# Optimization experiments

Hardware: AMD Instinct MI355X
Metric: run time of the kernel (lower is better)

## Reference

```python
import jax, jax.numpy as jnp
import numpy as np

D_MODEL = 1024
N_HEADS = 16
HEAD_DIM = D_MODEL // N_HEADS


def setup_inputs() -> dict:
    key = jax.random.key(0)
    ks = jax.random.split(key, 9)
    B, S = 2, 2048
    s = 1.0 / np.sqrt(D_MODEL)
    return {
        "x": jax.random.normal(ks[0], (B, S, D_MODEL), dtype=jnp.float32),
        "Wq": jax.random.normal(ks[1], (D_MODEL, D_MODEL), dtype=jnp.float32) * s,
        "bq": jnp.zeros((D_MODEL,), dtype=jnp.float32),
        "Wk": jax.random.normal(ks[2], (D_MODEL, D_MODEL), dtype=jnp.float32) * s,
        "bk": jnp.zeros((D_MODEL,), dtype=jnp.float32),
        "Wv": jax.random.normal(ks[3], (D_MODEL, D_MODEL), dtype=jnp.float32) * s,
        "bv": jnp.zeros((D_MODEL,), dtype=jnp.float32),
        "Wo": jax.random.normal(ks[4], (D_MODEL, D_MODEL), dtype=jnp.float32) * s,
        "bo": jnp.zeros((D_MODEL,), dtype=jnp.float32),
    }


def _rope_emb(seq_len, dtype):
    # inv_freq over even dims of head_dim; emb = cat(freqs, freqs)
    inv_freq = 1.0 / (10000.0 ** (jnp.arange(0, HEAD_DIM, 2, dtype=jnp.float32) / HEAD_DIM))
    t = jnp.arange(seq_len, dtype=jnp.float32)
    freqs = t[:, None] * inv_freq[None, :]          # [S, head_dim/2]
    emb = jnp.concatenate([freqs, freqs], axis=-1)  # [S, head_dim]
    return emb.astype(dtype)[None, None, :, :]       # [1,1,S,head_dim]


def _rotate_half(x):
    x1, x2 = jnp.split(x, 2, axis=-1)
    return jnp.concatenate([-x2, x1], axis=-1)


def _apply_rope(x, emb):
    return x * jnp.cos(emb) + _rotate_half(x) * jnp.sin(emb)


def reference(x, Wq, bq, Wk, bk, Wv, bv, Wo, bo):
    B, S, _ = x.shape
    # projections (torch Linear: x @ W.T + b; here W is stored already as [in,out])
    q = (x @ Wq + bq).reshape(B, S, N_HEADS, HEAD_DIM).transpose(0, 2, 1, 3)
    k = (x @ Wk + bk).reshape(B, S, N_HEADS, HEAD_DIM).transpose(0, 2, 1, 3)
    v = (x @ Wv + bv).reshape(B, S, N_HEADS, HEAD_DIM).transpose(0, 2, 1, 3)
    emb = _rope_emb(S, x.dtype)
    q = _apply_rope(q, emb)
    k = _apply_rope(k, emb)
    scores = jnp.einsum('bhqd,bhkd->bhqk', q, k) / jnp.sqrt(jnp.asarray(HEAD_DIM, x.dtype))
    attn = jax.nn.softmax(scores, axis=-1)
    out = jnp.einsum('bhqk,bhkd->bhqd', attn, v)
    out = out.transpose(0, 2, 1, 3).reshape(B, S, D_MODEL)
    return out @ Wo + bo
```

## Files before the change

### kernel.cpp

```cpp
#include <hip/hip_runtime.h>
#include <hip/hip_bf16.h>
#include <math.h>

#define SEQ 2048
#define DM 1024
#define NH 16
#define HD 64
#define NBH 32
#define MTOT 4096

typedef __attribute__((ext_vector_type(8))) short short8;
typedef __attribute__((ext_vector_type(4))) float floatx4;
typedef __attribute__((ext_vector_type(8))) unsigned short u16x8;

__device__ __forceinline__ unsigned short f2bf(float f) {
    unsigned int u = __float_as_uint(f);
    u += 0x7FFFu + ((u >> 16) & 1u);
    return (unsigned short)(u >> 16);
}

#define AS1C const __attribute__((address_space(1))) void*
#define AS3  __attribute__((address_space(3))) void*

#define QSCALE 0.18033688011112042f

__global__ __launch_bounds__(256) void cvt_x_kernel(
    const float* __restrict__ x, unsigned short* __restrict__ xb)
{
    size_t base = ((size_t)blockIdx.x * 256 + threadIdx.x) * 8;
    float4 a = *(const float4*)(x + base);
    float4 b = *(const float4*)(x + base + 4);
    u16x8 o;
    o[0]=f2bf(a.x); o[1]=f2bf(a.y); o[2]=f2bf(a.z); o[3]=f2bf(a.w);
    o[4]=f2bf(b.x); o[5]=f2bf(b.y); o[6]=f2bf(b.z); o[7]=f2bf(b.w);
    *(u16x8*)(xb + base) = o;
}

__global__ __launch_bounds__(256) void cvt_w_kernel(
    const float* __restrict__ Wq, const float* __restrict__ Wk,
    const float* __restrict__ Wv, const float* __restrict__ Wo,
    unsigned short* __restrict__ Wt)
{
    __shared__ float Ls[64][65];
    const int z = blockIdx.z;
    const float* src = (z==0) ? Wq : (z==1) ? Wk : (z==2) ? Wv : Wo;
    unsigned short* dst = Wt + (size_t)z * DM * DM;
    const int tid = threadIdx.x;
    const int k0 = blockIdx.x * 64, n0 = blockIdx.y * 64;

    int r = tid >> 2, cseg = (tid & 3) * 16;
    #pragma unroll
    for (int e = 0; e < 4; ++e) {
        float4 v = *(const float4*)(src + (size_t)(k0 + r) * DM + n0 + cseg + e*4);
        Ls[r][cseg+e*4+0] = v.x; Ls[r][cseg+e*4+1] = v.y;
        Ls[r][cseg+e*4+2] = v.z; Ls[r][cseg+e*4+3] = v.w;
    }
    __syncthreads();
    int n = tid >> 2, kseg = (tid & 3) * 16;
    #pragma unroll
    for (int half = 0; half < 2; ++half) {
        u16x8 o;
        #pragma unroll
        for (int e = 0; e < 8; ++e) o[e] = f2bf(Ls[kseg + half*8 + e][n]);
        *(u16x8*)(dst + (size_t)(n0 + n) * DM + k0 + kseg + half*8) = o;
    }
}

#define GEMM_CORE(A_, Bt_, m0_, n0_)                                          \
    const int tid = threadIdx.x;                                              \
    const int wave = tid >> 6, lane = tid & 63;                               \
    const int quad = lane >> 4, l16 = lane & 15;                              \
    const int mh = (wave & 1) * 64, nh = (wave >> 1) * 64;                    \
    floatx4 acc[4][4];                                                        \
    _Pragma("unroll")                                                         \
    for (int i = 0; i < 4; ++i)                                               \
        _Pragma("unroll")                                                     \
        for (int j = 0; j < 4; ++j) acc[i][j] = (floatx4){0.f,0.f,0.f,0.f};   \
    {                                                                         \
        const int srow = wave*32 + (lane>>2);                                 \
        const int scol = (lane & 3) * 8;                                      \
        const unsigned short* ga = A_ + (size_t)(m0_ + srow)*DM + scol;       \
        const unsigned short* gb = Bt_ + (size_t)(n0_ + srow)*DM + scol;      \
        char* lA = (char*)As; char* lB = (char*)Bs;                           \
        for (int k0 = 0; k0 < DM; k0 += 32) {                                 \
            __syncthreads();                                                  \
            _Pragma("unroll")                                                 \
            for (int u = 0; u < 2; ++u) {                                     \
                __builtin_amdgcn_global_load_lds(                             \
                    (AS1C)(ga + (size_t)u*16*DM + k0),                        \
                    (AS3)(lA + (wave*32 + u*16)*64), 16, 0, 0);               \
                __builtin_amdgcn_global_load_lds(                             \
                    (AS1C)(gb + (size_t)u*16*DM + k0),                        \
                    (AS3)(lB + (wave*32 + u*16)*64), 16, 0, 0);               \
            }                                                                 \
            __syncthreads();                                                  \
            short8 af[4], bf[4];                                              \
            _Pragma("unroll")                                                 \
            for (int t = 0; t < 4; ++t) {                                     \
                af[t] = *(const short8*)&As[(mh + t*16 + l16)*32 + quad*8];   \
                bf[t] = *(const short8*)&Bs[(nh + t*16 + l16)*32 + quad*8];   \
            }                                                                 \
            _Pragma("unroll")                                                 \
            for (int mt = 0; mt < 4; ++mt)                                    \
                _Pragma("unroll")                                             \
                for (int nt = 0; nt < 4; ++nt)                                \
                    acc[mt][nt] = __builtin_amdgcn_mfma_f32_16x16x32_bf16(    \
                        af[mt], bf[nt], acc[mt][nt], 0, 0, 0);                \
        }                                                                     \
    }

__global__ __launch_bounds__(256, 3) void qkv_gemm_kernel(
    const unsigned short* __restrict__ xb, const unsigned short* __restrict__ Wt,
    const float* __restrict__ bq, const float* __restrict__ bk,
    const float* __restrict__ bv,
    unsigned short* __restrict__ qb, unsigned short* __restrict__ kb,
    unsigned short* __restrict__ vtg)
{
    __shared__ unsigned short As[128*32];
    __shared__ unsigned short Bs[128*32];
    const int z = blockIdx.z;
    const unsigned short* Bt = Wt + (size_t)z * DM * DM;
    const float* bias = (z==0) ? bq : (z==1) ? bk : bv;
    const int m0 = blockIdx.x * 128, n0 = blockIdx.y * 128;

    GEMM_CORE(xb, Bt, m0, n0)

    float bb[4];
    #pragma unroll
    for (int nt = 0; nt < 4; ++nt) bb[nt] = bias[n0 + nh + nt*16 + l16];

    if (z == 2) {
        unsigned short* Tw = (wave & 1) ? Bs : As;
        const int b = m0 >> 11;
        const int bufsel = tid >> 7, nl = tid & 127;
        const int ng = n0 + nl, hh = ng >> 6, dhh = ng & 63;
        unsigned short* vrow = vtg + ((size_t)((b*NH + hh)*HD + dhh))*SEQ;
        #pragma unroll
        for (int t = 0; t < 4; ++t) {
            __syncthreads();
            #pragma unroll
            for (int nt = 0; nt < 4; ++nt)
                #pragma unroll
                for (int r = 0; r < 4; ++r)
                    Tw[(nh + nt*16 + l16)*24 + quad*4 + r] =
                        f2bf(acc[t][nt][r] + bb[nt]);
            __syncthreads();
            const unsigned short* T2 = bufsel ? Bs : As;
            int sbase = (m0 & 2047) + bufsel*64 + t*16;
            u16x8 lo = *(const u16x8*)&T2[nl*24];
            u16x8 hi = *(const u16x8*)&T2[nl*24 + 8];
            *(u16x8*)(vrow + sbase)     = lo;
            *(u16x8*)(vrow + sbase + 8) = hi;
        }
    } else {
        unsigned short* outh = (z==0) ? qb : kb;
        const float scl = (z == 0) ? QSCALE : 1.0f;
        float inv[2];
        #pragma unroll
        for (int p = 0; p < 2; ++p)
            inv[p] = __expf(-(float)(p*16 + l16) * 0.28782313662425572f);
        #pragma unroll
        for (int mt = 0; mt < 4; ++mt)
            #pragma unroll
            for (int r = 0; r < 4; ++r) {
                int m = m0 + mh + mt*16 + quad*4 + r;
                int b = m >> 11, s = m & (SEQ-1);
                #pragma unroll
                for (int p = 0; p < 2; ++p) {
                    float fr = (float)s * inv[p];
                    float sn, c; __sincosf(fr, &sn, &c);
                    int n1 = n0 + nh + p*16 + l16;
                    int h = n1 >> 6, dh = n1 & 63;
                    float v1 = acc[mt][p  ][r] + bb[p];
                    float v2 = acc[mt][p+2][r] + bb[p+2];
                    unsigned short* base = outh + ((size_t)(b*NH + h)*SEQ + s)*HD;
                    base[dh]      = f2bf((v1*c - v2*sn) * scl);
                    base[dh + 32] = f2bf((v2*c + v1*sn) * scl);
                }
            }
    }
}

__global__ __launch_bounds__(256, 3) void out_gemm_kernel(
    const unsigned short* __restrict__ ctxb, const unsigned short* __restrict__ Wto,
    const float* __restrict__ bo, float* __restrict__ outf)
{
    __shared__ unsigned short As[128*32];
    __shared__ unsigned short Bs[128*32];
    const int m0 = blockIdx.x * 128, n0 = blockIdx.y * 128;

    GEMM_CORE(ctxb, Wto, m0, n0)

    float bb[4];
    #pragma unroll
    for (int nt = 0; nt < 4; ++nt) bb[nt] = bo[n0 + nh + nt*16 + l16];
    #pragma unroll
    for (int mt = 0; mt < 4; ++mt)
        #pragma unroll
        for (int r = 0; r < 4; ++r) {
            int m = m0 + mh + mt*16 + quad*4 + r;
            #pragma unroll
            for (int nt = 0; nt < 4; ++nt) {
                int n = n0 + nh + nt*16 + l16;
                outf[(size_t)m*DM + n] = acc[mt][nt][r] + bb[nt];
            }
        }
}

#define LSTP 72
__global__ __launch_bounds__(512, 4) void attn_mfma_kernel(
    const unsigned short* __restrict__ Q, const unsigned short* __restrict__ K,
    const unsigned short* __restrict__ Vtg, unsigned short* __restrict__ ctxb)
{
    __shared__ unsigned short Ks[2*64*32];
    __shared__ unsigned short Vt[2*64*32];
    __shared__ unsigned short Ps[8*16*LSTP];

    const int tid  = threadIdx.x;
    const int wave = tid >> 6, lane = tid & 63;
    const int quad = lane >> 4, l16 = lane & 15;
    const int qt = blockIdx.x, bh = blockIdx.y;

    const unsigned short* Qb = Q + (size_t)bh * SEQ * HD;
    const unsigned short* Kb = K + (size_t)bh * SEQ * HD;
    const unsigned short* Vb = Vtg + (size_t)bh * HD * SEQ;

    short8 qf[2];
    {
        const unsigned short* qrow = Qb + (size_t)(qt*128 + wave*16 + l16)*HD;
        qf[0] = *(const short8*)(qrow + quad*8);
        qf[1] = *(const short8*)(qrow + 32 + quad*8);
    }

    const unsigned short* gsrc0; const unsigned short* gsrc1;
    char* ldst0; char* ldst1;
    int step;
    {
        const int ib = (wave & 3) * 2;
        int f0 = (ib+0)*512 + lane*8;
        int f1 = (ib+1)*512 + lane*8;
        int ch0 = f0>>11, row0 = (f0&2047)>>5, g0 = ((f0>>3)&3) ^ (row0&3);
        int ch1 = f1>>11, row1 = (f1&2047)>>5, g1 = ((f1>>3)&3) ^ (row1&3);
        if (wave < 4) {
            gsrc0 = Kb + (size_t)row0*HD + ch0*32 + g0*8;
            gsrc1 = Kb + (size_t)row1*HD + ch1*32 + g1*8;
            ldst0 = (char*)Ks + (ib+0)*1024;
            ldst1 = (char*)Ks + (ib+1)*1024;
            step = 64*HD;
        } else {
            gsrc0 = Vb + (size_t)row0*SEQ + ch0*32 + g0*8;
            gsrc1 = Vb + (size_t)row1*SEQ + ch1*32 + g1*8;
            ldst0 = (char*)Vt + (ib+0)*1024;
            ldst1 = (char*)Vt + (ib+1)*1024;
            step = 64;
        }
    }

    float l_i[4];
    floatx4 Oacc[4];
    #pragma unroll
    for (int r = 0; r < 4; ++r) l_i[r] = 0.f;
    #pragma unroll
    for (int dt = 0; dt < 4; ++dt) Oacc[dt] = (floatx4){0.f,0.f,0.f,0.f};

    const int swz8 = (quad ^ (l16&3)) * 8;

    for (int kt = 0; kt < SEQ/64; ++kt) {
        __syncthreads();
        __builtin_amdgcn_global_load_lds((AS1C)gsrc0, (AS3)ldst0, 16, 0, 0);
        __builtin_amdgcn_global_load_lds((AS1C)gsrc1, (AS3)ldst1, 16, 0, 0);
        gsrc0 += step; gsrc1 += step;
        __syncthreads();

        floatx4 Sacc[4];
        #pragma unroll
        for (int c = 0; c < 4; ++c) Sacc[c] = (floatx4){0.f,0.f,0.f,0.f};
        #pragma unroll
        for (int s = 0; s < 2; ++s) {
            #pragma unroll
            for (int c = 0; c < 4; ++c) {
                short8 b = *(const short8*)&Ks[s*2048 + (c*16+l16)*32 + swz8];
                Sacc[c] = __builtin_amdgcn_mfma_f32_16x16x32_bf16(qf[s], b, Sacc[c], 0, 0, 0);
            }
        }

        #pragma unroll
        for (int r = 0; r < 4; ++r) {
            float p0 = exp2f(Sacc[0][r]);
            float p1 = exp2f(Sacc[1][r]);
            float p2 = exp2f(Sacc[2][r]);
            float p3 = exp2f(Sacc[3][r]);
            l_i[r] += (p0 + p1) + (p2 + p3);
            __hip_bfloat162 w0 = __float22bfloat162_rn(make_float2(p0, p1));
            __hip_bfloat162 w1 = __float22bfloat162_rn(make_float2(p2, p3));
            unsigned short* prow = &Ps[(wave*16 + quad*4 + r)*LSTP + l16];
            __builtin_memcpy(&prow[0],  &w0.x, 2);
            __builtin_memcpy(&prow[16], &w0.y, 2);
            __builtin_memcpy(&prow[32], &w1.x, 2);
            __builtin_memcpy(&prow[48], &w1.y, 2);
        }

        #pragma unroll
        for (int s = 0; s < 2; ++s) {
            short8 a = *(const short8*)&Ps[(wave*16 + l16)*LSTP + s*32 + quad*8];
            #pragma unroll
            for (int dt = 0; dt < 4; ++dt) {
                short8 b = *(const short8*)&Vt[s*2048 + (dt*16+l16)*32 + swz8];
                Oacc[dt] = __builtin_amdgcn_mfma_f32_16x16x32_bf16(a, b, Oacc[dt], 0, 0, 0);
            }
        }
    }

    #pragma unroll
    for (int mask = 1; mask < 16; mask <<= 1)
        #pragma unroll
        for (int r = 0; r < 4; ++r)
            l_i[r] += __shfl_xor(l_i[r], mask);

    int b = bh >> 4, h = bh & 15;
    #pragma unroll
    for (int r = 0; r < 4; ++r) {
        int sr = qt*128 + wave*16 + quad*4 + r;
        float invl = 1.0f / l_i[r];
        unsigned short* dst = ctxb + ((size_t)(b*SEQ + sr))*DM + h*HD;
        #pragma unroll
        for (int dt = 0; dt < 4; ++dt)
            dst[dt*16 + l16] = f2bf(Oacc[dt][r] * invl);
    }
}

extern "C" void kernel_launch(void* const* d_in, const int* in_sizes, int n_in,
                              void* d_out, int out_size, void* d_ws, size_t ws_size,
                              hipStream_t stream) {
    const float* x  = (const float*)d_in[0];
    const float* Wq = (const float*)d_in[1];
    const float* bq = (const float*)d_in[2];
    const float* Wk = (const float*)d_in[3];
    const float* bk = (const float*)d_in[4];
    const float* Wv = (const float*)d_in[5];
    const float* bv = (const float*)d_in[6];
    const float* Wo = (const float*)d_in[7];
    const float* bo = (const float*)d_in[8];
    float* out = (float*)d_out;

    char* ws = (char*)d_ws;
    unsigned short* xb   = (unsigned short*)(ws);
    unsigned short* Wt   = (unsigned short*)(ws +  8u*1024*1024);
    unsigned short* qb   = (unsigned short*)(ws + 16u*1024*1024);
    unsigned short* kb   = (unsigned short*)(ws + 24u*1024*1024);
    unsigned short* vtg  = (unsigned short*)(ws + 32u*1024*1024);
    unsigned short* ctxb = (unsigned short*)(ws + 40u*1024*1024);

    cvt_x_kernel<<<(MTOT*DM/8)/256, 256, 0, stream>>>(x, xb);
    cvt_w_kernel<<<dim3(DM/64, DM/64, 4), 256, 0, stream>>>(Wq, Wk, Wv, Wo, Wt);

    qkv_gemm_kernel<<<dim3(MTOT/128, DM/128, 3), 256, 0, stream>>>(
        xb, Wt, bq, bk, bv, qb, kb, vtg);

    attn_mfma_kernel<<<dim3(SEQ/128, NBH), 512, 0, stream>>>(qb, kb, vtg, ctxb);

    out_gemm_kernel<<<dim3(MTOT/128, DM/128), 256, 0, stream>>>(
        ctxb, Wt + (size_t)3*DM*DM, bo, out);
    (void)in_sizes; (void)n_in; (void)out_size; (void)ws_size;
}
```

Before: 216.0 us.

## Widen attention key tile to 128, permute Q/K head layout, vectorize RoPE stores

The attention kernel now processes 128 keys per iteration instead of 64. This halves the number of barrier-separated load phases, and the P matrix is permuted in LDS to match. The QKV epilogue writes Q/K with a permuted head-dim layout (pairs interleaved), so each lane emits one 8-byte vector store instead of scattered 2-byte stores. This works because the dot product is invariant when Q and K are permuted the same way. The grid is flattened so the 32 heads of one query tile launch adjacently. The larger tile raises LDS and register use, which could lower occupancy.

Measured after the change: 212.0 us. No clear change (-1.8%).

```diff
diff --git a/kernel.cpp b/kernel.cpp
--- a/kernel.cpp
+++ b/kernel.cpp
@@ -12,6 +12,7 @@
 typedef __attribute__((ext_vector_type(8))) short short8;
 typedef __attribute__((ext_vector_type(4))) float floatx4;
 typedef __attribute__((ext_vector_type(8))) unsigned short u16x8;
+typedef __attribute__((ext_vector_type(4))) unsigned short u16x4;
 
 __device__ __forceinline__ unsigned short f2bf(float f) {
     unsigned int u = __float_as_uint(f);
@@ -155,28 +156,28 @@
     } else {
         unsigned short* outh = (z==0) ? qb : kb;
         const float scl = (z == 0) ? QSCALE : 1.0f;
-        float inv[2];
-        #pragma unroll
-        for (int p = 0; p < 2; ++p)
-            inv[p] = __expf(-(float)(p*16 + l16) * 0.28782313662425572f);
+        const int h = (n0 + nh) >> 6;
+        float inv0 = __expf(-(float)l16        * 0.28782313662425572f);
+        float inv1 = __expf(-(float)(l16 + 16) * 0.28782313662425572f);
         #pragma unroll
         for (int mt = 0; mt < 4; ++mt)
             #pragma unroll
             for (int r = 0; r < 4; ++r) {
                 int m = m0 + mh + mt*16 + quad*4 + r;
                 int b = m >> 11, s = m & (SEQ-1);
-                #pragma unroll
-                for (int p = 0; p < 2; ++p) {
-                    float fr = (float)s * inv[p];
-                    float sn, c; __sincosf(fr, &sn, &c);
-                    int n1 = n0 + nh + p*16 + l16;
-                    int h = n1 >> 6, dh = n1 & 63;
-                    float v1 = acc[mt][p  ][r] + bb[p];
-                    float v2 = acc[mt][p+2][r] + bb[p+2];
-                    unsigned short* base = outh + ((size_t)(b*NH + h)*SEQ + s)*HD;
-                    base[dh]      = f2bf((v1*c - v2*sn) * scl);
-                    base[dh + 32] = f2bf((v2*c + v1*sn) * scl);
-                }
+                float s0, c0, s1, c1;
+                __sincosf((float)s * inv0, &s0, &c0);
+                __sincosf((float)s * inv1, &s1, &c1);
+                float a0 = acc[mt][0][r] + bb[0];
+                float a1 = acc[mt][1][r] + bb[1];
+                float a2 = acc[mt][2][r] + bb[2];
+                float a3 = acc[mt][3][r] + bb[3];
+                u16x4 o;
+                o[0] = f2bf((a0*c0 - a2*s0) * scl);
+                o[1] = f2bf((a1*c1 - a3*s1) * scl);
+                o[2] = f2bf((a2*c0 + a0*s0) * scl);
+                o[3] = f2bf((a3*c1 + a1*s1) * scl);
+                *(u16x4*)(outh + ((size_t)((b*NH + h)*SEQ + s))*HD + 4*l16) = o;
             }
     }
 }
@@ -212,14 +213,15 @@
     const unsigned short* __restrict__ Q, const unsigned short* __restrict__ K,
     const unsigned short* __restrict__ Vtg, unsigned short* __restrict__ ctxb)
 {
-    __shared__ unsigned short Ks[2*64*32];
-    __shared__ unsigned short Vt[2*64*32];
+    __shared__ unsigned short Ks[2*128*32];
+    __shared__ unsigned short Vt[4*64*32];
     __shared__ unsigned short Ps[8*16*LSTP];
 
     const int tid  = threadIdx.x;
     const int wave = tid >> 6, lane = tid & 63;
     const int quad = lane >> 4, l16 = lane & 15;
-    const int qt = blockIdx.x, bh = blockIdx.y;
+    const int bh = blockIdx.x & 31;
+    const int qt = blockIdx.x >> 5;
 
     const unsigned short* Qb = Q + (size_t)bh * SEQ * HD;
     const unsigned short* Kb = K + (size_t)bh * SEQ * HD;
@@ -232,27 +234,31 @@
         qf[1] = *(const short8*)(qrow + 32 + quad*8);
     }
 
-    const unsigned short* gsrc0; const unsigned short* gsrc1;
-    char* ldst0; char* ldst1;
+    const unsigned short* gsrc[4];
+    char* ldst[4];
     int step;
     {
-        const int ib = (wave & 3) * 2;
-        int f0 = (ib+0)*512 + lane*8;
-        int f1 = (ib+1)*512 + lane*8;
-        int ch0 = f0>>11, row0 = (f0&2047)>>5, g0 = ((f0>>3)&3) ^ (row0&3);
-        int ch1 = f1>>11, row1 = (f1&2047)>>5, g1 = ((f1>>3)&3) ^ (row1&3);
+        const int idx = (wave & 3)*64 + lane;
         if (wave < 4) {
-            gsrc0 = Kb + (size_t)row0*HD + ch0*32 + g0*8;
-            gsrc1 = Kb + (size_t)row1*HD + ch1*32 + g1*8;
-            ldst0 = (char*)Ks + (ib+0)*1024;
-            ldst1 = (char*)Ks + (ib+1)*1024;
-            step = 64*HD;
+            #pragma unroll
+            for (int u = 0; u < 4; ++u) {
+                int fI = u*2048 + idx*8;
+                int s  = fI >> 12, rm = fI & 4095;
+                int key = rm >> 5, g = ((rm >> 3) & 3) ^ (key & 3);
+                gsrc[u] = Kb + (size_t)key*HD + s*32 + g*8;
+                ldst[u] = (char*)Ks + (u*2048 + (wave & 3)*512)*2;
+            }
+            step = 128*HD;
         } else {
-            gsrc0 = Vb + (size_t)row0*SEQ + ch0*32 + g0*8;
-            gsrc1 = Vb + (size_t)row1*SEQ + ch1*32 + g1*8;
-            ldst0 = (char*)Vt + (ib+0)*1024;
-            ldst1 = (char*)Vt + (ib+1)*1024;
-            step = 64;
+            #pragma unroll
+            for (int u = 0; u < 4; ++u) {
+                int fI = u*2048 + idx*8;
+                int ch = fI >> 11, rm = fI & 2047;
+                int d = rm >> 5, g = ((rm >> 3) & 3) ^ (d & 3);
+                gsrc[u] = Vb + (size_t)d*SEQ + ch*32 + g*8;
+                ldst[u] = (char*)Vt + (u*2048 + (wave & 3)*512)*2;
+            }
+            step = 128;
         }
     }
 
@@ -263,50 +269,57 @@
     #pragma unroll
     for (int dt = 0; dt < 4; ++dt) Oacc[dt] = (floatx4){0.f,0.f,0.f,0.f};
 
-    const int swz8 = (quad ^ (l16&3)) * 8;
-
-    for (int kt = 0; kt < SEQ/64; ++kt) {
+    const int swz8 = (quad ^ (l16 & 3)) * 8;
+    const int physr = ((l16 >> 2) << 1) + ((l16 & 1) << 3) + ((l16 & 2) >> 1);
+    const unsigned short* parow = &Ps[(wave*16 + physr)*LSTP];
+    unsigned short* pwbase = &Ps[(wave*16 + quad*2)*LSTP + l16];
+
+    for (int kt = 0; kt < SEQ/128; ++kt) {
         __syncthreads();
-        __builtin_amdgcn_global_load_lds((AS1C)gsrc0, (AS3)ldst0, 16, 0, 0);
-        __builtin_amdgcn_global_load_lds((AS1C)gsrc1, (AS3)ldst1, 16, 0, 0);
-        gsrc0 += step; gsrc1 += step;
+        #pragma unroll
+        for (int u = 0; u < 4; ++u)
+            __builtin_amdgcn_global_load_lds((AS1C)gsrc[u], (AS3)ldst[u], 16, 0, 0);
+        #pragma unroll
+        for (int u = 0; u < 4; ++u) gsrc[u] += step;
         __syncthreads();
 
-        floatx4 Sacc[4];
-        #pragma unroll
-        for (int c = 0; c < 4; ++c) Sacc[c] = (floatx4){0.f,0.f,0.f,0.f};
+        floatx4 Sacc[8];
+        #pragma unroll
+        for (int c = 0; c < 8; ++c) Sacc[c] = (floatx4){0.f,0.f,0.f,0.f};
         #pragma unroll
         for (int s = 0; s < 2; ++s) {
             #pragma unroll
-            for (int c = 0; c < 4; ++c) {
-                short8 b = *(const short8*)&Ks[s*2048 + (c*16+l16)*32 + swz8];
+            for (int c = 0; c < 8; ++c) {
+                short8 b = *(const short8*)&Ks[s*4096 + (c*16 + l16)*32 + swz8];
                 Sacc[c] = __builtin_amdgcn_mfma_f32_16x16x32_bf16(qf[s], b, Sacc[c], 0, 0, 0);
             }
         }
 
         #pragma unroll
-        for (int r = 0; r < 4; ++r) {
-            float p0 = exp2f(Sacc[0][r]);
-            float p1 = exp2f(Sacc[1][r]);
-            float p2 = exp2f(Sacc[2][r]);
-            float p3 = exp2f(Sacc[3][r]);
-            l_i[r] += (p0 + p1) + (p2 + p3);
-            __hip_bfloat162 w0 = __float22bfloat162_rn(make_float2(p0, p1));
-            __hip_bfloat162 w1 = __float22bfloat162_rn(make_float2(p2, p3));
-            unsigned short* prow = &Ps[(wave*16 + quad*4 + r)*LSTP + l16];
-            __builtin_memcpy(&prow[0],  &w0.x, 2);
-            __builtin_memcpy(&prow[16], &w0.y, 2);
-            __builtin_memcpy(&prow[32], &w1.x, 2);
-            __builtin_memcpy(&prow[48], &w1.y, 2);
-        }
-
-        #pragma unroll
-        for (int s = 0; s < 2; ++s) {
-            short8 a = *(const short8*)&Ps[(wave*16 + l16)*LSTP + s*32 + quad*8];
-            #pragma unroll
-            for (int dt = 0; dt < 4; ++dt) {
-                short8 b = *(const short8*)&Vt[s*2048 + (dt*16+l16)*32 + swz8];
-                Oacc[dt] = __builtin_amdgcn_mfma_f32_16x16x32_bf16(a, b, Oacc[dt], 0, 0, 0);
+        for (int h = 0; h < 2; ++h) {
+            #pragma unroll
+            for (int r = 0; r < 4; ++r) {
+                float p0 = exp2f(Sacc[h*4+0][r]);
+                float p1 = exp2f(Sacc[h*4+1][r]);
+                float p2 = exp2f(Sacc[h*4+2][r]);
+                float p3 = exp2f(Sacc[h*4+3][r]);
+                l_i[r] += (p0 + p1) + (p2 + p3);
+                __hip_bfloat162 w0 = __float22bfloat162_rn(make_float2(p0, p1));
+                __hip_bfloat162 w1 = __float22bfloat162_rn(make_float2(p2, p3));
+                unsigned short* prow = pwbase + (((r & 1) << 3) + (r >> 1))*LSTP;
+                __builtin_memcpy(&prow[0],  &w0.x, 2);
+                __builtin_memcpy(&prow[16], &w0.y, 2);
+                __builtin_memcpy(&prow[32], &w1.x, 2);
+                __builtin_memcpy(&prow[48], &w1.y, 2);
+            }
+            #pragma unroll
+            for (int s = 0; s < 2; ++s) {
+                short8 a = *(const short8*)(parow + s*32 + quad*8);
+                #pragma unroll
+                for (int dt = 0; dt < 4; ++dt) {
+                    short8 b = *(const short8*)&Vt[(h*2+s)*2048 + (dt*16+l16)*32 + swz8];
+                    Oacc[dt] = __builtin_amdgcn_mfma_f32_16x16x32_bf16(a, b, Oacc[dt], 0, 0, 0);
+                }
             }
         }
     }
@@ -357,7 +370,7 @@
     qkv_gemm_kernel<<<dim3(MTOT/128, DM/128, 3), 256, 0, stream>>>(
         xb, Wt, bq, bk, bv, qb, kb, vtg);
 
-    attn_mfma_kernel<<<dim3(SEQ/128, NBH), 512, 0, stream>>>(qb, kb, vtg, ctxb);
+    attn_mfma_kernel<<<512, 512, 0, stream>>>(qb, kb, vtg, ctxb);
 
     out_gemm_kernel<<<dim3(MTOT/128, DM/128), 256, 0, stream>>>(
         ctxb, Wt + (size_t)3*DM*DM, bo, out);
```
